# Performance work log

Measured on AMD Instinct MI355X. Metric: run time of the kernel, lower is better.

Reference implementation:

```python
import jax, jax.numpy as jnp
import numpy as np

K = 1          # self.k: number of hardest positives kept per row
MARGIN = 0.1   # self.margin


def setup_inputs() -> dict:
    key = jax.random.key(0)
    n, d, n_classes = 8192, 512, 1024  # 8 samples per class (balanced, as the torch reshape assumes)
    inputs = jax.random.normal(key, (n, d), dtype=jnp.float32)
    targets = (jnp.arange(n) % n_classes).astype(jnp.int32)
    return {"inputs": inputs, "targets": targets}


def _euclidean_dist(x):
    # ||xi||^2 + ||xj||^2 - 2 xi.xj, clamped then sqrt (matches torch addmm_ version)
    sq = jnp.sum(x * x, axis=1)
    d2 = sq[:, None] + sq[None, :] - 2.0 * (x @ x.T)
    return jnp.sqrt(jnp.clip(d2, 1e-12))


def reference(inputs, targets):
    n = inputs.shape[0]
    dist = _euclidean_dist(inputs)                      # [n, n]

    same = targets[:, None] == targets[None, :]
    eye = jnp.eye(n, dtype=bool)
    pos_mask = same & ~eye                              # same label, excl. diagonal
    neg_mask = ~same                                    # different label

    inf = jnp.asarray(jnp.inf, dist.dtype)
    # per-row sorted positive distances (non-positives pushed to +inf)
    pos_sorted = jnp.sort(jnp.where(pos_mask, dist, inf), axis=1)
    topk_pos = pos_sorted[:, :K]                        # k closest positives per row
    mean_pos = jnp.mean(topk_pos, axis=1)               # mean(pos_pair[:k])
    thresh = pos_sorted[:, K - 1] + MARGIN              # pos_pair[-1] + margin

    # hard negatives: neg distance < threshold
    sel = neg_mask & (dist < thresh[:, None])
    cnt = jnp.sum(sel, axis=1)
    sum_neg = jnp.sum(jnp.where(sel, dist, 0.0), axis=1)
    mean_neg = sum_neg / jnp.maximum(cnt, 1).astype(dist.dtype)

    valid = cnt > 0
    row_loss = jnp.where(valid, mean_pos - mean_neg + MARGIN, 0.0)
    loss = jnp.sum(row_loss) / n

    prec = 1.0 - jnp.sum(valid).astype(dist.dtype) / n
    pos_d = jnp.sum(jnp.where(pos_mask, dist, 0.0)) / jnp.sum(pos_mask).astype(dist.dtype)
    neg_d = jnp.sum(jnp.where(neg_mask, dist, 0.0)) / jnp.sum(neg_mask).astype(dist.dtype)
    return loss, prec, pos_d, neg_d
```

## Files before the change

kernel.cpp:

```cpp
#include <hip/hip_runtime.h>
#include <hip/hip_bf16.h>
#include <math.h>


#define MARGIN_F 0.1f

typedef unsigned short ushort_t;
typedef __attribute__((ext_vector_type(8))) _Float16 f16x8;
typedef __attribute__((ext_vector_type(4))) float f32x4;

__global__ void nl_prep_kernel(const float* __restrict__ x, float* __restrict__ sq,
                               ushort_t* __restrict__ xh,
                               float* __restrict__ neg_total, unsigned int* __restrict__ neg_cnt,
                               int n, int d) {
  int row = blockIdx.x * blockDim.y + threadIdx.y;
  if (row >= n) return;
  const float* xr = x + (size_t)row * d;
  float s = 0.f;
  for (int k = threadIdx.x * 4; k < d; k += 64 * 4) {
    float4 v = *reinterpret_cast<const float4*>(xr + k);
    s = fmaf(v.x, v.x, s); s = fmaf(v.y, v.y, s);
    s = fmaf(v.z, v.z, s); s = fmaf(v.w, v.w, s);
    if (xh != nullptr) {
      float f[4] = {v.x, v.y, v.z, v.w};
      union { ushort_t u[4]; uint2 v2; } H;
#pragma unroll
      for (int t = 0; t < 4; ++t) {
        _Float16 h = (_Float16)f[t];
        H.u[t] = *reinterpret_cast<ushort_t*>(&h);
      }
      *reinterpret_cast<uint2*>(xh + (size_t)row * d + k) = H.v2;
    }
  }
#pragma unroll
  for (int off = 32; off > 0; off >>= 1) s += __shfl_down(s, off, 64);
  if (threadIdx.x == 0) sq[row] = s;
  if (row == 0 && threadIdx.x == 0) { *neg_total = 0.f; *neg_cnt = 0u; }
}

__launch_bounds__(1024)
__global__ void nl_bucket_kernel(const int* __restrict__ targets,
                                 int* __restrict__ cls_start, int* __restrict__ members,
                                 int n) {
  __shared__ int cnt[8192];
  __shared__ int aux[1024];
  const int tid = threadIdx.x;
  for (int k = tid; k < n; k += 1024) cnt[k] = 0;
  __syncthreads();
  for (int k = tid; k < n; k += 1024) atomicAdd(&cnt[targets[k]], 1);
  __syncthreads();
  const int C = (n + 1023) / 1024;
  int v[8]; int s = 0;
  for (int e = 0; e < C; ++e) {
    int idx = tid * C + e;
    int t = (idx < n) ? cnt[idx] : 0;
    v[e] = s; s += t;
  }
  aux[tid] = s;
  __syncthreads();
  for (int off = 1; off < 1024; off <<= 1) {
    int t = (tid >= off) ? aux[tid - off] : 0;
    __syncthreads();
    aux[tid] += t;
    __syncthreads();
  }
  int chunk_excl = aux[tid] - s;
  __syncthreads();
  for (int e = 0; e < C; ++e) {
    int idx = tid * C + e;
    if (idx < n) {
      int st = chunk_excl + v[e];
      cls_start[idx] = st;
      cnt[idx] = st;
    }
  }
  __syncthreads();
  for (int k = tid; k < n; k += 1024) {
    int t = targets[k];
    int p = atomicAdd(&cnt[t], 1);
    members[p] = k;
  }
}

__launch_bounds__(256)
__global__ void nl_pos_bucket(const float* __restrict__ x, const int* __restrict__ targets,
                              const float* __restrict__ sq,
                              const int* __restrict__ cls_start, const int* __restrict__ members,
                              float* __restrict__ min_pos, float* __restrict__ pos_sum,
                              int* __restrict__ pos_cnt,
                              float* __restrict__ sel_sum, int* __restrict__ sel_cnt,
                              int n, int d) {
  const int lane = threadIdx.x & 63;
  const int i = (blockIdx.x * blockDim.x + threadIdx.x) >> 6;
  if (i >= n) return;
  const int tgt = targets[i];
  const float sqi = sq[i];
  const float* xi = x + (size_t)i * d;
  float4 xreg[2];
  const int k0 = lane * 4;
#pragma unroll
  for (int c = 0; c < 2; ++c)
    if (k0 + c * 256 < d) xreg[c] = *reinterpret_cast<const float4*>(xi + k0 + c * 256);
  const int s = cls_start[tgt];
  const int e = (tgt + 1 < n) ? cls_start[tgt + 1] : n;
  float mn = INFINITY, sum = 0.f;
  int cnt = 0;
  for (int mi = s; mi < e; ++mi) {
    int j = members[mi];
    if (j == i) continue;
    const float* xj = x + (size_t)j * d;
    float acc = 0.f;
    if (d == 512) {
      float4 a0 = xreg[0], a1 = xreg[1];
      float4 v0 = *reinterpret_cast<const float4*>(xj + k0);
      float4 v1 = *reinterpret_cast<const float4*>(xj + k0 + 256);
      acc = fmaf(a0.x, v0.x, acc); acc = fmaf(a0.y, v0.y, acc);
      acc = fmaf(a0.z, v0.z, acc); acc = fmaf(a0.w, v0.w, acc);
      acc = fmaf(a1.x, v1.x, acc); acc = fmaf(a1.y, v1.y, acc);
      acc = fmaf(a1.z, v1.z, acc); acc = fmaf(a1.w, v1.w, acc);
    } else {
      for (int k = k0; k < d; k += 256) {
        float4 a = *reinterpret_cast<const float4*>(xi + k);
        float4 v = *reinterpret_cast<const float4*>(xj + k);
        acc = fmaf(a.x, v.x, acc); acc = fmaf(a.y, v.y, acc);
        acc = fmaf(a.z, v.z, acc); acc = fmaf(a.w, v.w, acc);
      }
    }
#pragma unroll
    for (int off = 32; off > 0; off >>= 1) acc += __shfl_down(acc, off, 64);
    if (lane == 0) {
      float d2 = sqi + sq[j] - 2.f * acc;
      float dist = sqrtf(fmaxf(d2, 1e-12f));
      mn = fminf(mn, dist); sum += dist; cnt++;
    }
  }
  if (lane == 0) {
    min_pos[i] = mn; pos_sum[i] = sum; pos_cnt[i] = cnt;
    sel_sum[i] = 0.f; sel_cnt[i] = 0;
  }
}

__launch_bounds__(256)
__global__ void nl_pos_scan(const float* __restrict__ x, const int* __restrict__ targets,
                            const float* __restrict__ sq,
                            float* __restrict__ min_pos, float* __restrict__ pos_sum,
                            int* __restrict__ pos_cnt,
                            float* __restrict__ sel_sum, int* __restrict__ sel_cnt,
                            int n, int d) {
  const int lane = threadIdx.x & 63;
  const int i = (blockIdx.x * blockDim.x + threadIdx.x) >> 6;
  if (i >= n) return;
  const int tgt = targets[i];
  const float sqi = sq[i];
  const float* xi = x + (size_t)i * d;
  float mn = INFINITY, sum = 0.f;
  int cnt = 0;
  for (int j0 = 0; j0 < n; j0 += 64) {
    int j = j0 + lane;
    bool match = (j < n) && (j != i) && (targets[j] == tgt);
    unsigned long long mask = __ballot(match);
    while (mask) {
      int b = __ffsll(mask) - 1;
      mask &= mask - 1;
      int jj = j0 + b;
      const float* xj = x + (size_t)jj * d;
      float acc = 0.f;
      for (int k = lane * 4; k < d; k += 256) {
        float4 a = *reinterpret_cast<const float4*>(xi + k);
        float4 v = *reinterpret_cast<const float4*>(xj + k);
        acc = fmaf(a.x, v.x, acc); acc = fmaf(a.y, v.y, acc);
        acc = fmaf(a.z, v.z, acc); acc = fmaf(a.w, v.w, acc);
      }
#pragma unroll
      for (int off = 32; off > 0; off >>= 1) acc += __shfl_down(acc, off, 64);
      if (lane == 0) {
        float d2 = sqi + sq[jj] - 2.f * acc;
        float dist = sqrtf(fmaxf(d2, 1e-12f));
        mn = fminf(mn, dist); sum += dist; cnt++;
      }
    }
  }
  if (lane == 0) {
    min_pos[i] = mn; pos_sum[i] = sum; pos_cnt[i] = cnt;
    sel_sum[i] = 0.f; sel_cnt[i] = 0;
  }
}

__device__ __forceinline__ void stage_tile512(const ushort_t* __restrict__ S, int r0, int k0,
                                              int ld, char* lds) {
  const int c = threadIdx.x;
  int row = c >> 2;
  int kc = (c & 3) ^ ((row >> 1) & 3);
  const ushort_t* g = S + (size_t)(r0 + row) * ld + k0 + kc * 8;
  __builtin_amdgcn_global_load_lds(
      (const __attribute__((address_space(1))) unsigned int*)g,
      (__attribute__((address_space(3))) unsigned int*)(lds + c * 16),
      16, 0, 0);
}

__launch_bounds__(512, 6)
__global__ void nl_main_mfma(const ushort_t* __restrict__ xh,
                             const int* __restrict__ targets, const float* __restrict__ sq,
                             const float* __restrict__ min_pos,
                             float* __restrict__ sel_sum, int* __restrict__ sel_cnt,
                             float* __restrict__ neg_total, unsigned int* __restrict__ neg_cnt,
                             int n, int d) {
  __shared__ char smem[2][8192];
  __shared__ float red_sel[128];
  __shared__ int red_cnt[128];
  __shared__ float red_csel[128];
  __shared__ int red_ccnt[128];
  __shared__ float red_neg;
  __shared__ unsigned int red_negc;

  const int tid = threadIdx.x;
  const int lane = tid & 63;
  const int w = tid >> 6;
  const int wr = w >> 2, wc = w & 3;

  const int nwg = gridDim.x;
  const int q8 = nwg >> 3, r8 = nwg & 7;
  const int xcd = blockIdx.x & 7, sub = blockIdx.x >> 3;
  const int wg = (xcd < r8 ? xcd * (q8 + 1) : r8 * (q8 + 1) + (xcd - r8) * q8) + sub;

  const int nbx = n >> 7;
  int tt = wg, bi = 0, len = nbx;
  while (tt >= len) { tt -= len; ++bi; --len; }
  const int bj = bi + tt;
  const int row0 = bi * 128, col0 = bj * 128;
  const bool isdiag = (bi == bj);

  if (tid < 128) { red_sel[tid] = 0.f; red_cnt[tid] = 0; red_csel[tid] = 0.f; red_ccnt[tid] = 0; }
  if (tid == 0) { red_neg = 0.f; red_negc = 0u; }

  f32x4 acc[4][2];
#pragma unroll
  for (int m = 0; m < 4; ++m)
#pragma unroll
    for (int nn = 0; nn < 2; ++nn) acc[m][nn] = (f32x4){0.f, 0.f, 0.f, 0.f};

  const int TOT = d >> 5;

  stage_tile512(xh, row0, 0, d, smem[0]);
  stage_tile512(xh, col0, 0, d, smem[1]);

  const int r = lane & 15;
  const int g = lane >> 4;
  const int chunk = (g ^ ((r >> 1) & 3)) * 16;

  for (int kt = 0; kt < TOT; ++kt) {
    asm volatile("s_waitcnt vmcnt(0)" ::: "memory");
    __builtin_amdgcn_s_barrier();
    __builtin_amdgcn_sched_barrier(0);

    f16x8 a[4], b[2];
#pragma unroll
    for (int m = 0; m < 4; ++m)
      a[m] = *reinterpret_cast<const f16x8*>(smem[0] + (wr * 64 + m * 16 + r) * 64 + chunk);
#pragma unroll
    for (int nn = 0; nn < 2; ++nn)
      b[nn] = *reinterpret_cast<const f16x8*>(smem[1] + (wc * 32 + nn * 16 + r) * 64 + chunk);
#pragma unroll
    for (int m = 0; m < 4; ++m)
#pragma unroll
      for (int nn = 0; nn < 2; ++nn)
        acc[m][nn] = __builtin_amdgcn_mfma_f32_16x16x32_f16(a[m], b[nn], acc[m][nn], 0, 0, 0);

    if (kt + 1 < TOT) {
      asm volatile("s_waitcnt lgkmcnt(0)" ::: "memory");
      __builtin_amdgcn_s_barrier();
      __builtin_amdgcn_sched_barrier(0);
      int k0 = (kt + 1) << 5;
      stage_tile512(xh, row0, k0, d, smem[0]);
      stage_tile512(xh, col0, k0, d, smem[1]);
    }
  }

  const int col_base = col0 + wc * 32;
  float sqj[2], thrj[2];
  int tgtj[2];
#pragma unroll
  for (int nn = 0; nn < 2; ++nn) {
    int gc = col_base + nn * 16 + (lane & 15);
    sqj[nn] = sq[gc];
    tgtj[nn] = targets[gc];
    thrj[nn] = min_pos[gc] + MARGIN_F;
  }
  float negsum = 0.f;
  unsigned int negc = 0u;
  float colsum[2] = {0.f, 0.f};
  int colcnt[2] = {0, 0};
#pragma unroll
  for (int m = 0; m < 4; ++m) {
#pragma unroll
    for (int reg = 0; reg < 4; ++reg) {
      int lrow = wr * 64 + m * 16 + (lane >> 4) * 4 + reg;
      int gr = row0 + lrow;
      float sqi = sq[gr];
      int tgti = targets[gr];
      float thr = min_pos[gr] + MARGIN_F;
      float rs = 0.f; int rc = 0;
#pragma unroll
      for (int nn = 0; nn < 2; ++nn) {
        float d2 = sqi + sqj[nn] - 2.f * acc[m][nn][reg];
        float dist = sqrtf(fmaxf(d2, 1e-12f));
        if (tgti != tgtj[nn]) {
          negsum += dist; negc++;
          if (dist < thr) { rc++; rs += dist; }
          if (!isdiag && dist < thrj[nn]) { colcnt[nn]++; colsum[nn] += dist; }
        }
      }
#pragma unroll
      for (int off = 1; off < 16; off <<= 1) {
        rs += __shfl_xor(rs, off, 64);
        rc += __shfl_xor(rc, off, 64);
      }
      if ((lane & 15) == 0) {
        atomicAdd(&red_cnt[lrow], rc);
        atomicAdd(&red_sel[lrow], rs);
      }
    }
  }
  if (!isdiag) {
#pragma unroll
    for (int nn = 0; nn < 2; ++nn) {
      float cs = colsum[nn]; int cc = colcnt[nn];
      cs += __shfl_xor(cs, 16, 64); cc += __shfl_xor(cc, 16, 64);
      cs += __shfl_xor(cs, 32, 64); cc += __shfl_xor(cc, 32, 64);
      if ((lane >> 4) == 0 && cc) {
        int lcol = wc * 32 + nn * 16 + lane;
        atomicAdd(&red_ccnt[lcol], cc);
        atomicAdd(&red_csel[lcol], cs);
      }
    }
    negsum *= 2.f; negc *= 2u;
  }
#pragma unroll
  for (int off = 32; off > 0; off >>= 1) {
    negsum += __shfl_down(negsum, off, 64);
    negc += __shfl_down(negc, off, 64);
  }
  if (lane == 0) { atomicAdd(&red_neg, negsum); atomicAdd(&red_negc, negc); }
  __syncthreads();
  if (tid < 128) {
    int c = red_cnt[tid];
    if (c > 0) {
      atomicAdd(&sel_cnt[row0 + tid], c);
      atomicAdd(&sel_sum[row0 + tid], red_sel[tid]);
    }
    if (!isdiag) {
      int c2 = red_ccnt[tid];
      if (c2 > 0) {
        atomicAdd(&sel_cnt[col0 + tid], c2);
        atomicAdd(&sel_sum[col0 + tid], red_csel[tid]);
      }
    }
  }
  if (tid == 0) { atomicAdd(neg_total, red_neg); atomicAdd(neg_cnt, red_negc); }
}

#define BM 128
#define BN 128
#define BK 16
#define PAD 4
__launch_bounds__(256)
__global__ void nl_main_kernel(const float* __restrict__ x, const int* __restrict__ targets,
                               const float* __restrict__ sq, const float* __restrict__ min_pos,
                               float* __restrict__ sel_sum, int* __restrict__ sel_cnt,
                               float* __restrict__ neg_total, unsigned int* __restrict__ neg_cnt,
                               int n, int d) {
  __shared__ float As[BK][BM + PAD];
  __shared__ float Bs[BK][BN + PAD];
  __shared__ float red_sel[BM];
  __shared__ int red_cnt[BM];
  __shared__ float red_neg;
  __shared__ unsigned int red_negc;

  const int tid = threadIdx.x;
  const int tx = tid & 15;
  const int ty = tid >> 4;
  const int row0 = blockIdx.y * BM;
  const int col0 = blockIdx.x * BN;

  if (tid < BM) { red_sel[tid] = 0.f; red_cnt[tid] = 0; }
  if (tid == 0) { red_neg = 0.f; red_negc = 0u; }

  float acc[8][8];
#pragma unroll
  for (int i = 0; i < 8; ++i)
#pragma unroll
    for (int j = 0; j < 8; ++j) acc[i][j] = 0.f;

  const int lr = tid >> 2;
  const int lk = (tid & 3) << 2;

  for (int k0 = 0; k0 < d; k0 += BK) {
    float4 va0 = *reinterpret_cast<const float4*>(x + (size_t)(row0 + lr) * d + k0 + lk);
    float4 va1 = *reinterpret_cast<const float4*>(x + (size_t)(row0 + lr + 64) * d + k0 + lk);
    float4 vb0 = *reinterpret_cast<const float4*>(x + (size_t)(col0 + lr) * d + k0 + lk);
    float4 vb1 = *reinterpret_cast<const float4*>(x + (size_t)(col0 + lr + 64) * d + k0 + lk);
    __syncthreads();
    As[lk + 0][lr] = va0.x; As[lk + 1][lr] = va0.y; As[lk + 2][lr] = va0.z; As[lk + 3][lr] = va0.w;
    As[lk + 0][lr + 64] = va1.x; As[lk + 1][lr + 64] = va1.y; As[lk + 2][lr + 64] = va1.z; As[lk + 3][lr + 64] = va1.w;
    Bs[lk + 0][lr] = vb0.x; Bs[lk + 1][lr] = vb0.y; Bs[lk + 2][lr] = vb0.z; Bs[lk + 3][lr] = vb0.w;
    Bs[lk + 0][lr + 64] = vb1.x; Bs[lk + 1][lr + 64] = vb1.y; Bs[lk + 2][lr + 64] = vb1.z; Bs[lk + 3][lr + 64] = vb1.w;
    __syncthreads();
#pragma unroll
    for (int k = 0; k < BK; ++k) {
      float a[8], b[8];
      *reinterpret_cast<float4*>(&a[0]) = *reinterpret_cast<const float4*>(&As[k][ty * 4]);
      *reinterpret_cast<float4*>(&a[4]) = *reinterpret_cast<const float4*>(&As[k][ty * 4 + 64]);
      *reinterpret_cast<float4*>(&b[0]) = *reinterpret_cast<const float4*>(&Bs[k][tx * 4]);
      *reinterpret_cast<float4*>(&b[4]) = *reinterpret_cast<const float4*>(&Bs[k][tx * 4 + 64]);
#pragma unroll
      for (int mm = 0; mm < 8; ++mm)
#pragma unroll
        for (int nn = 0; nn < 8; ++nn)
          acc[mm][nn] = fmaf(a[mm], b[nn], acc[mm][nn]);
    }
  }

  float sqj[8]; int tgtj[8];
#pragma unroll
  for (int nn = 0; nn < 8; ++nn) {
    int lc = tx * 4 + (nn & 3) + ((nn >> 2) << 6);
    sqj[nn] = sq[col0 + lc];
    tgtj[nn] = targets[col0 + lc];
  }
  float negsum = 0.f;
  unsigned int negc = 0u;
#pragma unroll
  for (int mm = 0; mm < 8; ++mm) {
    int lrow = ty * 4 + (mm & 3) + ((mm >> 2) << 6);
    int gi = row0 + lrow;
    float sqi = sq[gi];
    int tgti = targets[gi];
    float thr = min_pos[gi] + MARGIN_F;
    float rs = 0.f; int rc = 0;
#pragma unroll
    for (int nn = 0; nn < 8; ++nn) {
      float d2 = sqi + sqj[nn] - 2.f * acc[mm][nn];
      float dist = sqrtf(fmaxf(d2, 1e-12f));
      if (tgti != tgtj[nn]) {
        negsum += dist; negc++;
        if (dist < thr) { rc++; rs += dist; }
      }
    }
    if (rc) { atomicAdd(&red_cnt[lrow], rc); atomicAdd(&red_sel[lrow], rs); }
  }
#pragma unroll
  for (int off = 32; off > 0; off >>= 1) {
    negsum += __shfl_down(negsum, off, 64);
    negc += __shfl_down(negc, off, 64);
  }
  if ((tid & 63) == 0) { atomicAdd(&red_neg, negsum); atomicAdd(&red_negc, negc); }
  __syncthreads();
  if (tid < BM && red_cnt[tid] > 0) {
    atomicAdd(&sel_cnt[row0 + tid], red_cnt[tid]);
    atomicAdd(&sel_sum[row0 + tid], red_sel[tid]);
  }
  if (tid == 0) { atomicAdd(neg_total, red_neg); atomicAdd(neg_cnt, red_negc); }
}

__global__ void nl_finalize(const float* __restrict__ min_pos, const float* __restrict__ pos_sum,
                            const int* __restrict__ pos_cnt, const float* __restrict__ sel_sum,
                            const int* __restrict__ sel_cnt, const float* __restrict__ neg_total,
                            const unsigned int* __restrict__ neg_cnt, float* __restrict__ out,
                            int n) {
  const int tid = threadIdx.x;
  float loss = 0.f, psum = 0.f;
  int nvalid = 0, pcnt = 0;
  for (int i = tid; i < n; i += 256) {
    int c = sel_cnt[i];
    if (c > 0) {
      float mean_neg = sel_sum[i] / (float)c;
      loss += min_pos[i] - mean_neg + MARGIN_F;
      nvalid++;
    }
    psum += pos_sum[i];
    pcnt += pos_cnt[i];
  }
  __shared__ float s_loss[256];
  __shared__ float s_psum[256];
  __shared__ int s_nv[256];
  __shared__ int s_pc[256];
  s_loss[tid] = loss; s_psum[tid] = psum; s_nv[tid] = nvalid; s_pc[tid] = pcnt;
  __syncthreads();
  for (int s = 128; s > 0; s >>= 1) {
    if (tid < s) {
      s_loss[tid] += s_loss[tid + s];
      s_psum[tid] += s_psum[tid + s];
      s_nv[tid] += s_nv[tid + s];
      s_pc[tid] += s_pc[tid + s];
    }
    __syncthreads();
  }
  if (tid == 0) {
    out[0] = s_loss[0] / (float)n;
    out[1] = 1.f - (float)s_nv[0] / (float)n;
    out[2] = s_psum[0] / (float)s_pc[0];
    out[3] = neg_total[0] / (float)neg_cnt[0];
  }
}

extern "C" void kernel_launch(void* const* d_in, const int* in_sizes, int n_in,
                              void* d_out, int out_size, void* d_ws, size_t ws_size,
                              hipStream_t stream) {
  const float* x = (const float*)d_in[0];
  const int* targets = (const int*)d_in[1];
  float* out = (float*)d_out;
  const int n = in_sizes[1];
  const int d = in_sizes[0] / n;

  float* sq = (float*)d_ws;
  float* min_pos = sq + n;
  float* pos_sum = min_pos + n;
  int* pos_cnt = (int*)(pos_sum + n);
  float* sel_sum = (float*)(pos_cnt + n);
  int* sel_cnt = (int*)(sel_sum + n);
  int* cls_start = (int*)(sel_cnt + n);
  int* members = cls_start + n;
  float* neg_total = (float*)(members + n);
  unsigned int* neg_cnt = (unsigned int*)(neg_total + 1);
  size_t stats_bytes = ((size_t)(8 * n + 2) * 4 + 255) & ~(size_t)255;
  ushort_t* xh = (ushort_t*)((char*)d_ws + stats_bytes);
  size_t need = stats_bytes + (size_t)n * d * sizeof(ushort_t);

  const bool mfma_ok = (ws_size >= need) && (n % 128) == 0 && (d % 32) == 0;
  const bool bucket_ok = (ws_size >= stats_bytes) && (n <= 8192) && (d % 16) == 0;

  nl_prep_kernel<<<dim3((n + 3) / 4), dim3(64, 4), 0, stream>>>(
      x, sq, mfma_ok ? xh : nullptr, neg_total, neg_cnt, n, d);
  if (bucket_ok) {
    nl_bucket_kernel<<<1, 1024, 0, stream>>>(targets, cls_start, members, n);
    nl_pos_bucket<<<(n * 64 + 255) / 256, 256, 0, stream>>>(
        x, targets, sq, cls_start, members, min_pos, pos_sum, pos_cnt, sel_sum, sel_cnt, n, d);
  } else {
    nl_pos_scan<<<(n * 64 + 255) / 256, 256, 0, stream>>>(
        x, targets, sq, min_pos, pos_sum, pos_cnt, sel_sum, sel_cnt, n, d);
  }

  if (mfma_ok) {
    int nbx = n / 128;
    int ntiles = nbx * (nbx + 1) / 2;
    nl_main_mfma<<<ntiles, 512, 0, stream>>>(xh, targets, sq, min_pos, sel_sum,
                                             sel_cnt, neg_total, neg_cnt, n, d);
  } else {
    nl_main_kernel<<<dim3(n / BN, n / BM), 256, 0, stream>>>(x, targets, sq, min_pos, sel_sum,
                                                             sel_cnt, neg_total, neg_cnt, n, d);
  }
  nl_finalize<<<1, 256, 0, stream>>>(min_pos, pos_sum, pos_cnt, sel_sum, sel_cnt,
                                     neg_total, neg_cnt, out, n);
}
```

Baseline: 161.4 us.

## Compute positive-pair distances per class with shared-memory staging and symmetric pairs

Replaces the per-row positive-distance kernel with a per-class kernel: one 64-thread block per class loads all members' rows into LDS once, then computes each unordered pair's dot product once and updates both members' min and sum. This is meant to remove redundant global loads of the same class rows and halve the pairwise dot products. It launches n blocks, most of which exit immediately because only 1024 classes are non-empty. The pair loop is serialized within one wave per class, and a fallback path handles large classes.

```diff
diff --git a/kernel.cpp b/kernel.cpp
--- a/kernel.cpp
+++ b/kernel.cpp
@@ -82,61 +82,83 @@
   }
 }
 
-__launch_bounds__(256)
-__global__ void nl_pos_bucket(const float* __restrict__ x, const int* __restrict__ targets,
-                              const float* __restrict__ sq,
-                              const int* __restrict__ cls_start, const int* __restrict__ members,
-                              float* __restrict__ min_pos, float* __restrict__ pos_sum,
-                              int* __restrict__ pos_cnt,
-                              float* __restrict__ sel_sum, int* __restrict__ sel_cnt,
-                              int n, int d) {
-  const int lane = threadIdx.x & 63;
-  const int i = (blockIdx.x * blockDim.x + threadIdx.x) >> 6;
-  if (i >= n) return;
-  const int tgt = targets[i];
-  const float sqi = sq[i];
-  const float* xi = x + (size_t)i * d;
-  float4 xreg[2];
-  const int k0 = lane * 4;
-#pragma unroll
-  for (int c = 0; c < 2; ++c)
-    if (k0 + c * 256 < d) xreg[c] = *reinterpret_cast<const float4*>(xi + k0 + c * 256);
-  const int s = cls_start[tgt];
-  const int e = (tgt + 1 < n) ? cls_start[tgt + 1] : n;
-  float mn = INFINITY, sum = 0.f;
-  int cnt = 0;
-  for (int mi = s; mi < e; ++mi) {
-    int j = members[mi];
-    if (j == i) continue;
-    const float* xj = x + (size_t)j * d;
-    float acc = 0.f;
-    if (d == 512) {
-      float4 a0 = xreg[0], a1 = xreg[1];
-      float4 v0 = *reinterpret_cast<const float4*>(xj + k0);
-      float4 v1 = *reinterpret_cast<const float4*>(xj + k0 + 256);
-      acc = fmaf(a0.x, v0.x, acc); acc = fmaf(a0.y, v0.y, acc);
-      acc = fmaf(a0.z, v0.z, acc); acc = fmaf(a0.w, v0.w, acc);
-      acc = fmaf(a1.x, v1.x, acc); acc = fmaf(a1.y, v1.y, acc);
-      acc = fmaf(a1.z, v1.z, acc); acc = fmaf(a1.w, v1.w, acc);
-    } else {
-      for (int k = k0; k < d; k += 256) {
-        float4 a = *reinterpret_cast<const float4*>(xi + k);
-        float4 v = *reinterpret_cast<const float4*>(xj + k);
-        acc = fmaf(a.x, v.x, acc); acc = fmaf(a.y, v.y, acc);
-        acc = fmaf(a.z, v.z, acc); acc = fmaf(a.w, v.w, acc);
-      }
-    }
-#pragma unroll
-    for (int off = 32; off > 0; off >>= 1) acc += __shfl_down(acc, off, 64);
-    if (lane == 0) {
-      float d2 = sqi + sq[j] - 2.f * acc;
-      float dist = sqrtf(fmaxf(d2, 1e-12f));
-      mn = fminf(mn, dist); sum += dist; cnt++;
-    }
-  }
-  if (lane == 0) {
-    min_pos[i] = mn; pos_sum[i] = sum; pos_cnt[i] = cnt;
-    sel_sum[i] = 0.f; sel_cnt[i] = 0;
+__launch_bounds__(64)
+__global__ void nl_pos_class(const float* __restrict__ x, const float* __restrict__ sq,
+                             const int* __restrict__ cls_start, const int* __restrict__ members,
+                             float* __restrict__ min_pos, float* __restrict__ pos_sum,
+                             int* __restrict__ pos_cnt,
+                             float* __restrict__ sel_sum, int* __restrict__ sel_cnt,
+                             int n, int d) {
+  __shared__ float xr[16][512];
+  __shared__ float mnL[16], sumL[16];
+  const int c = blockIdx.x;
+  const int s = cls_start[c];
+  const int e = (c + 1 < n) ? cls_start[c + 1] : n;
+  const int cnt = e - s;
+  if (cnt <= 0) return;
+  const int lane = threadIdx.x;
+
+  if (cnt <= 16 && d <= 512) {
+    for (int m = 0; m < cnt; ++m) {
+      const float* row = x + (size_t)members[s + m] * d;
+      for (int k = lane * 4; k < d; k += 256)
+        *reinterpret_cast<float4*>(&xr[m][k]) = *reinterpret_cast<const float4*>(row + k);
+    }
+    if (lane < 16) { mnL[lane] = INFINITY; sumL[lane] = 0.f; }
+    __builtin_amdgcn_s_barrier();
+    for (int a = 0; a < cnt; ++a) {
+      for (int b = a + 1; b < cnt; ++b) {
+        float acc = 0.f;
+        for (int k = lane * 4; k < d; k += 256) {
+          float4 va = *reinterpret_cast<const float4*>(&xr[a][k]);
+          float4 vb = *reinterpret_cast<const float4*>(&xr[b][k]);
+          acc = fmaf(va.x, vb.x, acc); acc = fmaf(va.y, vb.y, acc);
+          acc = fmaf(va.z, vb.z, acc); acc = fmaf(va.w, vb.w, acc);
+        }
+#pragma unroll
+        for (int off = 32; off > 0; off >>= 1) acc += __shfl_xor(acc, off, 64);
+        if (lane == 0) {
+          int ia = members[s + a], ib = members[s + b];
+          float d2 = sq[ia] + sq[ib] - 2.f * acc;
+          float dist = sqrtf(fmaxf(d2, 1e-12f));
+          mnL[a] = fminf(mnL[a], dist); sumL[a] += dist;
+          mnL[b] = fminf(mnL[b], dist); sumL[b] += dist;
+        }
+      }
+    }
+    __builtin_amdgcn_s_barrier();
+    for (int m = lane; m < cnt; m += 64) {
+      int i = members[s + m];
+      min_pos[i] = mnL[m]; pos_sum[i] = sumL[m]; pos_cnt[i] = cnt - 1;
+      sel_sum[i] = 0.f; sel_cnt[i] = 0;
+    }
+  } else {
+    for (int a = 0; a < cnt; ++a) {
+      int i = members[s + a];
+      const float* xi = x + (size_t)i * d;
+      float mn = INFINITY, sum = 0.f;
+      for (int bm = 0; bm < cnt; ++bm) {
+        if (bm == a) continue;
+        int j = members[s + bm];
+        const float* xj = x + (size_t)j * d;
+        float acc = 0.f;
+        for (int k = lane * 4; k < d; k += 256) {
+          float4 va = *reinterpret_cast<const float4*>(xi + k);
+          float4 vb = *reinterpret_cast<const float4*>(xj + k);
+          acc = fmaf(va.x, vb.x, acc); acc = fmaf(va.y, vb.y, acc);
+          acc = fmaf(va.z, vb.z, acc); acc = fmaf(va.w, vb.w, acc);
+        }
+#pragma unroll
+        for (int off = 32; off > 0; off >>= 1) acc += __shfl_xor(acc, off, 64);
+        float d2 = sq[i] + sq[j] - 2.f * acc;
+        float dist = sqrtf(fmaxf(d2, 1e-12f));
+        mn = fminf(mn, dist); sum += dist;
+      }
+      if (lane == 0) {
+        min_pos[i] = mn; pos_sum[i] = sum; pos_cnt[i] = cnt - 1;
+        sel_sum[i] = 0.f; sel_cnt[i] = 0;
+      }
+    }
   }
 }
 
@@ -533,8 +555,8 @@
       x, sq, mfma_ok ? xh : nullptr, neg_total, neg_cnt, n, d);
   if (bucket_ok) {
     nl_bucket_kernel<<<1, 1024, 0, stream>>>(targets, cls_start, members, n);
-    nl_pos_bucket<<<(n * 64 + 255) / 256, 256, 0, stream>>>(
-        x, targets, sq, cls_start, members, min_pos, pos_sum, pos_cnt, sel_sum, sel_cnt, n, d);
+    nl_pos_class<<<n, 64, 0, stream>>>(
+        x, sq, cls_start, members, min_pos, pos_sum, pos_cnt, sel_sum, sel_cnt, n, d);
   } else {
     nl_pos_scan<<<(n * 64 + 255) / 256, 256, 0, stream>>>(
         x, targets, sq, min_pos, pos_sum, pos_cnt, sel_sum, sel_cnt, n, d);
```

After: 176.9 us. 9.6% more time.
